# Kernel optimization log

Hardware: AMD Instinct MI355X
Metric: run time of the kernel (lower is better)

The kernel has to match this reference:

```python
import jax, jax.numpy as jnp
import numpy as np

B, DIM, H, W = 4, 192, 128, 128
HEADS = 4
K_RATES = (1.0 / 2, 2.0 / 3, 3.0 / 4, 4.0 / 5)


def setup_inputs() -> dict:
    key = jax.random.key(0)
    ks = jax.random.split(key, 5)
    x = jax.random.normal(ks[0], (B, DIM, H, W), jnp.float32)
    w_qkv = jax.random.normal(ks[1], (3 * DIM, DIM, 1, 1), jnp.float32) * 0.05
    w_dw = jax.random.normal(ks[2], (3 * DIM, 1, 3, 3), jnp.float32) * 0.05
    w_proj = jax.random.normal(ks[3], (DIM, DIM, 1, 1), jnp.float32) * 0.05
    temperature = jnp.ones((HEADS, 1, 1), jnp.float32)
    attn_w = jnp.full((4,), 0.2, jnp.float32)
    return {"x": x, "w_qkv": w_qkv, "w_dw": w_dw, "w_proj": w_proj,
            "temperature": temperature, "attn_w": attn_w}


def _conv1x1(x, w):
    # x: [b,c,h,w], w: [o,c,1,1]
    return jnp.einsum('bchw,oc->bohw', x, w[:, :, 0, 0])


def _dwconv3x3(x, w):
    # depthwise 3x3, padding=1; w: [c,1,3,3]
    return jax.lax.conv_general_dilated(
        x, w, window_strides=(1, 1), padding=((1, 1), (1, 1)),
        dimension_numbers=('NCHW', 'OIHW', 'NCHW'),
        feature_group_count=x.shape[1])


def _l2norm(x, eps=1e-12):
    # matches F.normalize(dim=-1): x / max(||x||, eps)
    n = jnp.sqrt(jnp.sum(x * x, axis=-1, keepdims=True))
    return x / jnp.maximum(n, eps)


def reference(x, w_qkv, w_dw, w_proj, temperature, attn_w):
    b, c, h, w = x.shape
    qkv = _dwconv3x3(_conv1x1(x, w_qkv), w_dw)  # [b, 3c, h, w]
    q, k, v = jnp.split(qkv, 3, axis=1)

    def heads(t):
        return t.reshape(b, HEADS, c // HEADS, h * w)  # [b, head, C, hw]

    q, k, v = heads(q), heads(k), heads(v)
    q = _l2norm(q)
    k = _l2norm(k)

    C = q.shape[2]
    attn = jnp.einsum('bhcn,bhdn->bhcd', q, k) * temperature[None]  # [b,head,C,C]

    out = jnp.zeros_like(v)
    for i, rate in enumerate(K_RATES):
        k_val = max(1, int(C * rate))
        _, idx = jax.lax.top_k(attn, k_val)  # [b,head,C,k]
        mask = jax.nn.one_hot(idx, C, dtype=attn.dtype).sum(axis=-2)  # [b,head,C,C]
        branch = jnp.where(mask > 0, attn, -jnp.inf)
        branch = jax.nn.softmax(branch, axis=-1)
        out = out + jnp.einsum('bhcd,bhdn->bhcn', branch, v) * attn_w[i]

    out = out.reshape(b, c, h, w)
    return _conv1x1(out, w_proj)
```

## Files before the change

kernel.cpp:

```cpp
#include <hip/hip_runtime.h>
#include <math.h>
#include <stdint.h>

#define BB 4
#define DIM 192
#define HEADS 4
#define CH 48
#define HW 16384
#define C3 576
#define NCHUNK 64

typedef unsigned short ushort_t;
typedef __attribute__((ext_vector_type(8))) short short8;
typedef __attribute__((ext_vector_type(4))) float floatx4;

__device__ __forceinline__ float bf2f(unsigned int u) {
    union { unsigned int i; float f; } v; v.i = u << 16; return v.f;
}
__device__ __forceinline__ ushort_t f2bf(float f) {
    union { float f; unsigned int i; } v; v.f = f;
    unsigned int x = v.i;
    x += 0x7fffu + ((x >> 16) & 1u);
    return (ushort_t)(x >> 16);
}

__global__ __launch_bounds__(256) void zero_init(float* __restrict__ p, int n) {
    int i = blockIdx.x * 256 + threadIdx.x;
    if (i < n) p[i] = 0.f;
}

__global__ __launch_bounds__(256) void convert_split(
    const float* __restrict__ in, ushort_t* __restrict__ hi,
    ushort_t* __restrict__ lo, int n)
{
    int i = blockIdx.x * 256 + threadIdx.x;
    if (i < n) {
        float f = in[i];
        ushort_t h = f2bf(f);
        hi[i] = h;
        lo[i] = f2bf(f - bf2f(h));
    }
}

__global__ __launch_bounds__(256) void tconv(
    const float* __restrict__ in, ushort_t* __restrict__ out_hi,
    ushort_t* __restrict__ out_lo, long inStride)
{
    int z = blockIdx.z;
    in += (long)z * inStride;
    out_hi += (long)z * HW * DIM;
    out_lo += (long)z * HW * DIM;
    __shared__ ushort_t th[64][80];
    __shared__ ushort_t tl[64][80];
    int n0 = blockIdx.x * 64, k0 = blockIdx.y * 64;
    int t = threadIdx.x;
#pragma unroll
    for (int i = 0; i < 4; ++i) {
        int kl = (t >> 4) + 16 * i;
        float4 v = *(const float4*)(in + (long)(k0 + kl) * HW + n0 + (t & 15) * 4);
        int nl = (t & 15) * 4;
        ushort_t hx = f2bf(v.x), hy = f2bf(v.y), hz = f2bf(v.z), hw = f2bf(v.w);
        th[nl + 0][kl] = hx; th[nl + 1][kl] = hy;
        th[nl + 2][kl] = hz; th[nl + 3][kl] = hw;
        tl[nl + 0][kl] = f2bf(v.x - bf2f(hx));
        tl[nl + 1][kl] = f2bf(v.y - bf2f(hy));
        tl[nl + 2][kl] = f2bf(v.z - bf2f(hz));
        tl[nl + 3][kl] = f2bf(v.w - bf2f(hw));
    }
    __syncthreads();
#pragma unroll
    for (int i = 0; i < 2; ++i) {
        int nl = t >> 2, seg = (t & 3) + 4 * i;
        *(uint4*)(out_hi + (long)(n0 + nl) * DIM + k0 + seg * 8) = *(uint4*)&th[nl][seg * 8];
        *(uint4*)(out_lo + (long)(n0 + nl) * DIM + k0 + seg * 8) = *(uint4*)&tl[nl][seg * 8];
    }
}

__global__ __launch_bounds__(256) void tconv_b16(
    const ushort_t* __restrict__ in, ushort_t* __restrict__ out)
{
    int z = blockIdx.z;
    in  += (long)z * DIM * HW;
    out += (long)z * HW * DIM;
    __shared__ ushort_t th[64][80];
    int n0 = blockIdx.x * 64, k0 = blockIdx.y * 64;
    int t = threadIdx.x;
#pragma unroll
    for (int i = 0; i < 4; ++i) {
        int kl = (t >> 4) + 16 * i;
        uint2 v = *(const uint2*)(in + (long)(k0 + kl) * HW + n0 + (t & 15) * 4);
        int nl = (t & 15) * 4;
        th[nl + 0][kl] = (ushort_t)(v.x & 0xffffu);
        th[nl + 1][kl] = (ushort_t)(v.x >> 16);
        th[nl + 2][kl] = (ushort_t)(v.y & 0xffffu);
        th[nl + 3][kl] = (ushort_t)(v.y >> 16);
    }
    __syncthreads();
#pragma unroll
    for (int i = 0; i < 2; ++i) {
        int nl = t >> 2, seg = (t & 3) + 4 * i;
        *(uint4*)(out + (long)(n0 + nl) * DIM + k0 + seg * 8) = *(uint4*)&th[nl][seg * 8];
    }
}

#define BS_STRIDE 104
template<int TERMS>
__global__ __launch_bounds__(256) void gemm_reg(
    const ushort_t* __restrict__ Ahi, const ushort_t* __restrict__ Alo,
    const ushort_t* __restrict__ BThi, const ushort_t* __restrict__ BTlo,
    float* __restrict__ C, int M, int N,
    long strideA, long strideB, long strideC)
{
    int z = blockIdx.z;
    Ahi += z * strideA; Alo += z * strideA;
    BThi += z * strideB; BTlo += z * strideB;
    C += z * strideC;
    __shared__ ushort_t Bs0[64 * BS_STRIDE];
    __shared__ ushort_t Bs1[64 * BS_STRIDE];
    int t = threadIdx.x;
    int wave = t >> 6, lane = t & 63;
    int l15 = lane & 15, quad = lane >> 4;
    int m0 = blockIdx.y * 64, n0 = blockIdx.x * 64;
    int wm = (wave & 1) * 32, wn = (wave >> 1) * 32;
    floatx4 acc[2][2];
#pragma unroll
    for (int i = 0; i < 2; ++i)
#pragma unroll
        for (int j = 0; j < 2; ++j) acc[i][j] = (floatx4){0.f, 0.f, 0.f, 0.f};

    if (TERMS == 1) {
        short8 af[2][6];
#pragma unroll
        for (int mi = 0; mi < 2; ++mi)
#pragma unroll
            for (int k0 = 0; k0 < 6; ++k0)
                af[mi][k0] = *(const short8*)(Ahi
                    + (long)(m0 + wm + mi * 16 + l15) * 192 + k0 * 32 + quad * 8);
        for (int i = t; i < 1536; i += 256) {
            int r = i / 24, seg = i % 24;
            uint4 v = *(const uint4*)(BThi + (long)(n0 + r) * 192 + seg * 8);
            ushort_t* dst = (seg < 12) ? &Bs0[r * BS_STRIDE + seg * 8]
                                       : &Bs1[r * BS_STRIDE + (seg - 12) * 8];
            *(uint4*)dst = v;
        }
        __syncthreads();
#pragma unroll
        for (int k0 = 0; k0 < 6; ++k0) {
            int ks = k0 * 32 + quad * 8;
            const ushort_t* buf = (ks < 96) ? Bs0 : Bs1;
            int col = (ks < 96) ? ks : ks - 96;
            short8 bf[2];
#pragma unroll
            for (int ni = 0; ni < 2; ++ni)
                bf[ni] = *(const short8*)&buf[(wn + ni * 16 + l15) * BS_STRIDE + col];
#pragma unroll
            for (int mi = 0; mi < 2; ++mi)
#pragma unroll
                for (int ni = 0; ni < 2; ++ni)
                    acc[mi][ni] = __builtin_amdgcn_mfma_f32_16x16x32_bf16(
                        af[mi][k0], bf[ni], acc[mi][ni], 0, 0, 0);
        }
    } else {
#pragma unroll
        for (int kh = 0; kh < 2; ++kh) {
            short8 ah[2][3], al[2][3];
#pragma unroll
            for (int mi = 0; mi < 2; ++mi)
#pragma unroll
                for (int k0 = 0; k0 < 3; ++k0) {
                    long off = (long)(m0 + wm + mi * 16 + l15) * 192
                             + kh * 96 + k0 * 32 + quad * 8;
                    ah[mi][k0] = *(const short8*)(Ahi + off);
                    al[mi][k0] = *(const short8*)(Alo + off);
                }
            if (kh) __syncthreads();
            for (int i = t; i < 768; i += 256) {
                int r = i / 12, seg = i % 12;
                long goff = (long)(n0 + r) * 192 + kh * 96 + seg * 8;
                *(uint4*)&Bs0[r * BS_STRIDE + seg * 8] = *(const uint4*)(BThi + goff);
                *(uint4*)&Bs1[r * BS_STRIDE + seg * 8] = *(const uint4*)(BTlo + goff);
            }
            __syncthreads();
#pragma unroll
            for (int k0 = 0; k0 < 3; ++k0) {
                int col = k0 * 32 + quad * 8;
                short8 bh[2], bl[2];
#pragma unroll
                for (int ni = 0; ni < 2; ++ni) {
                    bh[ni] = *(const short8*)&Bs0[(wn + ni * 16 + l15) * BS_STRIDE + col];
                    bl[ni] = *(const short8*)&Bs1[(wn + ni * 16 + l15) * BS_STRIDE + col];
                }
#pragma unroll
                for (int mi = 0; mi < 2; ++mi)
#pragma unroll
                    for (int ni = 0; ni < 2; ++ni) {
                        acc[mi][ni] = __builtin_amdgcn_mfma_f32_16x16x32_bf16(
                            ah[mi][k0], bh[ni], acc[mi][ni], 0, 0, 0);
                        acc[mi][ni] = __builtin_amdgcn_mfma_f32_16x16x32_bf16(
                            ah[mi][k0], bl[ni], acc[mi][ni], 0, 0, 0);
                        acc[mi][ni] = __builtin_amdgcn_mfma_f32_16x16x32_bf16(
                            al[mi][k0], bh[ni], acc[mi][ni], 0, 0, 0);
                    }
            }
        }
    }
#pragma unroll
    for (int mi = 0; mi < 2; ++mi)
#pragma unroll
        for (int ni = 0; ni < 2; ++ni) {
            long base = (long)(m0 + wm + mi * 16 + quad * 4) * N + n0 + wn + ni * 16 + l15;
#pragma unroll
            for (int r = 0; r < 4; ++r)
                C[base + (long)r * N] = acc[mi][ni][r];
        }
}

__global__ __launch_bounds__(256) void dwconv3x3_lds(
    const float* __restrict__ in, const float* __restrict__ w,
    ushort_t* __restrict__ qk_hi, ushort_t* __restrict__ qk_lo,
    ushort_t* __restrict__ vbuf16, float* __restrict__ normsq,
    int c0, int chunk)
{
    __shared__ float tile[10][132];
    int z = blockIdx.z;
    int cl = blockIdx.y;
    int gc = c0 + cl;
    in  += (long)z * chunk * HW + (long)cl * HW;
    int y0 = blockIdx.x * 8;
    const float* wc = w + gc * 9;
    float wf[9];
#pragma unroll
    for (int i = 0; i < 9; ++i) wf[i] = wc[i];
    int t = threadIdx.x;
    if (t < 10) { tile[t][0] = 0.f; tile[t][129] = 0.f; }
    for (int i = t; i < 320; i += 256) {
        int r = i >> 5, c4 = (i & 31) * 4;
        int gy = y0 - 1 + r;
        float4 v = {0.f, 0.f, 0.f, 0.f};
        if (gy >= 0 && gy < 128) v = *(const float4*)(in + gy * 128 + c4);
        tile[r][1 + c4] = v.x; tile[r][2 + c4] = v.y;
        tile[r][3 + c4] = v.z; tile[r][4 + c4] = v.w;
    }
    __syncthreads();
    int yl = t >> 5, xl = (t & 31) * 4;
    float s0 = 0.f, s1 = 0.f, s2 = 0.f, s3 = 0.f;
#pragma unroll
    for (int r = 0; r < 3; ++r) {
        float c0v = tile[yl + r][xl + 0], c1v = tile[yl + r][xl + 1];
        float c2v = tile[yl + r][xl + 2], c3v = tile[yl + r][xl + 3];
        float c4v = tile[yl + r][xl + 4], c5v = tile[yl + r][xl + 5];
        float w0 = wf[r * 3], w1 = wf[r * 3 + 1], w2 = wf[r * 3 + 2];
        s0 += w0 * c0v + w1 * c1v + w2 * c2v;
        s1 += w0 * c1v + w1 * c2v + w2 * c3v;
        s2 += w0 * c2v + w1 * c3v + w2 * c4v;
        s3 += w0 * c3v + w1 * c4v + w2 * c5v;
    }
    long pix = (long)(y0 + yl) * 128 + xl;
    ushort_t h0 = f2bf(s0), h1 = f2bf(s1), h2 = f2bf(s2), h3 = f2bf(s3);
    uint2 ph;
    ph.x = (unsigned)h0 | ((unsigned)h1 << 16);
    ph.y = (unsigned)h2 | ((unsigned)h3 << 16);
    if (gc < 2 * DIM) {
        ushort_t l0 = f2bf(s0 - bf2f(h0)), l1 = f2bf(s1 - bf2f(h1));
        ushort_t l2 = f2bf(s2 - bf2f(h2)), l3 = f2bf(s3 - bf2f(h3));
        uint2 pl;
        pl.x = (unsigned)l0 | ((unsigned)l1 << 16);
        pl.y = (unsigned)l2 | ((unsigned)l3 << 16);
        long rbase = ((long)z * 384 + gc) * HW + pix;
        *(uint2*)(qk_hi + rbase) = ph;
        *(uint2*)(qk_lo + rbase) = pl;
        __syncthreads();
        float* red = (float*)tile;
        red[t] = s0 * s0 + s1 * s1 + s2 * s2 + s3 * s3;
        __syncthreads();
        for (int off = 128; off > 0; off >>= 1) {
            if (t < off) red[t] += red[t + off];
            __syncthreads();
        }
        if (t == 0) atomicAdd(&normsq[z * 512 + gc], red[0]);
    } else {
        *(uint2*)(vbuf16 + ((long)z * DIM + (gc - 2 * DIM)) * HW + pix) = ph;
    }
}

__global__ __launch_bounds__(256) void attn_mfma(
    const ushort_t* __restrict__ qk_hi, const ushort_t* __restrict__ qk_lo,
    float* __restrict__ partial)
{
    int z = blockIdx.z, h = blockIdx.y, pidx = blockIdx.x;
    int t = threadIdx.x;
    int wave = t >> 6, lane = t & 63;
    int l15 = lane & 15, quad = lane >> 4;
    long base = (long)z * 384 * HW;
    const ushort_t* qh = qk_hi + base + (long)(h * CH) * HW;
    const ushort_t* ql = qk_lo + base + (long)(h * CH) * HW;
    const ushort_t* kh = qk_hi + base + (long)(DIM + h * CH) * HW;
    const ushort_t* kl = qk_lo + base + (long)(DIM + h * CH) * HW;
    int ncol0 = pidx * 256 + wave * 64;

    floatx4 acc[3][3];
#pragma unroll
    for (int i = 0; i < 3; ++i)
#pragma unroll
        for (int j = 0; j < 3; ++j) acc[i][j] = (floatx4){0.f, 0.f, 0.f, 0.f};

#pragma unroll
    for (int ks = 0; ks < 2; ++ks) {
        int col = ncol0 + ks * 32 + quad * 8;
        short8 ah[3], al[3], bh[3], bl[3];
#pragma unroll
        for (int i = 0; i < 3; ++i) {
            long ro = (long)(i * 16 + l15) * HW + col;
            ah[i] = *(const short8*)(qh + ro);
            al[i] = *(const short8*)(ql + ro);
            bh[i] = *(const short8*)(kh + ro);
            bl[i] = *(const short8*)(kl + ro);
        }
#pragma unroll
        for (int mi = 0; mi < 3; ++mi)
#pragma unroll
            for (int ni = 0; ni < 3; ++ni) {
                acc[mi][ni] = __builtin_amdgcn_mfma_f32_16x16x32_bf16(
                    ah[mi], bh[ni], acc[mi][ni], 0, 0, 0);
                acc[mi][ni] = __builtin_amdgcn_mfma_f32_16x16x32_bf16(
                    ah[mi], bl[ni], acc[mi][ni], 0, 0, 0);
                acc[mi][ni] = __builtin_amdgcn_mfma_f32_16x16x32_bf16(
                    al[mi], bh[ni], acc[mi][ni], 0, 0, 0);
            }
    }

    __shared__ float sred[2][48 * 50];
    float* sb = sred[wave & 1];
    if (wave < 2) {
#pragma unroll
        for (int mi = 0; mi < 3; ++mi)
#pragma unroll
            for (int ni = 0; ni < 3; ++ni)
#pragma unroll
                for (int r = 0; r < 4; ++r)
                    sb[(mi * 16 + quad * 4 + r) * 50 + ni * 16 + l15] = acc[mi][ni][r];
    }
    __syncthreads();
    if (wave >= 2) {
#pragma unroll
        for (int mi = 0; mi < 3; ++mi)
#pragma unroll
            for (int ni = 0; ni < 3; ++ni)
#pragma unroll
                for (int r = 0; r < 4; ++r)
                    sb[(mi * 16 + quad * 4 + r) * 50 + ni * 16 + l15] += acc[mi][ni][r];
    }
    __syncthreads();
    float* pp = partial + ((long)(pidx * 16 + z * HEADS + h)) * 2304;
    for (int i = t; i < 2304; i += 256) {
        int row = i / 48, colo = i - row * 48;
        pp[i] = sred[0][row * 50 + colo] + sred[1][row * 50 + colo];
    }
}

__global__ __launch_bounds__(256) void topk_combine2(
    const float* __restrict__ partial, const float* __restrict__ normsq,
    const float* __restrict__ temp, const float* __restrict__ attn_w,
    float* __restrict__ Wc)
{
    int z = blockIdx.y;
    int wave = threadIdx.x >> 6, lane = threadIdx.x & 63;
    int rid = blockIdx.x * 4 + wave;
    int c = rid % CH, h = rid / CH;
    int d = lane;
    float a = -INFINITY;
    if (d < 48) {
        float s = 0.f;
        const float* pp = partial + (long)(z * HEADS + h) * 2304 + c * CH + d;
        for (int p = 0; p < NCHUNK; ++p) s += pp[(long)p * 16 * 2304];
        float invq = 1.0f / fmaxf(sqrtf(normsq[z * 512 + h * CH + c]), 1e-12f);
        float invk = 1.0f / fmaxf(sqrtf(normsq[z * 512 + DIM + h * CH + d]), 1e-12f);
        a = s * invq * invk * temp[h];
    }
    float m = a;
#pragma unroll
    for (int off = 32; off > 0; off >>= 1) m = fmaxf(m, __shfl_xor(m, off, 64));
    float e = (d < 48) ? expf(a - m) : 0.f;
    int rank = 0;
    for (int j = 0; j < 48; ++j) {
        float aj = __shfl(a, j, 64);
        rank += (aj > a) || (aj == a && j < d);
    }
    const int kv[4] = {24, 32, 36, 38};
    float s = 0.f;
#pragma unroll
    for (int i = 0; i < 4; ++i) {
        float contrib = (d < 48 && rank < kv[i]) ? e : 0.f;
#pragma unroll
        for (int off = 32; off > 0; off >>= 1) contrib += __shfl_xor(contrib, off, 64);
        s += (rank < kv[i]) ? attn_w[i] / contrib : 0.f;
    }
    if (d < 48) Wc[(long)z * 9216 + (long)rid * CH + d] = e * s;
}

__global__ __launch_bounds__(256) void build_m(
    const float* __restrict__ wproj, const float* __restrict__ Wc,
    ushort_t* __restrict__ Mb)
{
    int z = blockIdx.y;
    int idx = blockIdx.x * 256 + threadIdx.x;
    if (idx >= DIM * DIM) return;
    int cg = idx % DIM;
    int o  = idx / DIM;
    int h = cg / CH, d = cg % CH;
    const float* wp = wproj + o * DIM + h * CH;
    const float* wcc = Wc + (long)z * 9216 + (long)h * CH * CH + d;
    float s = 0.f;
#pragma unroll
    for (int ch = 0; ch < CH; ++ch) s += wp[ch] * wcc[ch * CH];
    Mb[(long)z * DIM * DIM + idx] = f2bf(s);
}

extern "C" void kernel_launch(void* const* d_in, const int* in_sizes, int n_in,
                              void* d_out, int out_size, void* d_ws, size_t ws_size,
                              hipStream_t stream) {
    const float* x      = (const float*)d_in[0];
    const float* w_qkv  = (const float*)d_in[1];
    const float* w_dw   = (const float*)d_in[2];
    const float* w_proj = (const float*)d_in[3];
    const float* temper = (const float*)d_in[4];
    const float* attn_w = (const float*)d_in[5];
    float* out = (float*)d_out;

    char* p = (char*)d_ws;
    ushort_t* qk_hi  = (ushort_t*)p;   p += (long)BB * 384 * HW * 2;
    ushort_t* qk_lo  = (ushort_t*)p;   p += (long)BB * 384 * HW * 2;
    ushort_t* vbuf16 = (ushort_t*)p;   p += (long)BB * DIM * HW * 2;
    ushort_t* xT_hi  = (ushort_t*)p;   p += (long)BB * HW * DIM * 2;
    ushort_t* xT_lo  = (ushort_t*)p;   p += (long)BB * HW * DIM * 2;
    ushort_t* wq_hi  = (ushort_t*)p;   p += (long)C3 * DIM * 2;
    ushort_t* wq_lo  = (ushort_t*)p;   p += (long)C3 * DIM * 2;
    float* normsq    = (float*)p;      p += (long)BB * 512 * 4;
    float* Wc        = (float*)p;      p += (long)BB * 9216 * 4;
    ushort_t* Mb     = (ushort_t*)p;   p += (long)BB * DIM * DIM * 2;
    float* pre       = (float*)p;
    float* partial   = pre;
    long avail = (long)ws_size - (long)(p - (char*)d_ws);
    int chunk = 64;
    if (avail >= (long)BB * 192 * HW * 4) chunk = 192;

    zero_init<<<(BB * 512 + 255) / 256, 256, 0, stream>>>(normsq, BB * 512);
    convert_split<<<(C3 * DIM + 255) / 256, 256, 0, stream>>>(
        w_qkv, wq_hi, wq_lo, C3 * DIM);
    tconv<<<dim3(HW / 64, DIM / 64, BB), 256, 0, stream>>>(
        x, xT_hi, xT_lo, (long)DIM * HW);

    for (int c0 = 0; c0 < C3; c0 += chunk) {
        if (c0 < 2 * DIM)
            gemm_reg<3><<<dim3(HW / 64, chunk / 64, BB), 256, 0, stream>>>(
                wq_hi + (long)c0 * DIM, wq_lo + (long)c0 * DIM, xT_hi, xT_lo,
                pre, chunk, HW, 0L, (long)HW * DIM, (long)chunk * HW);
        else
            gemm_reg<1><<<dim3(HW / 64, chunk / 64, BB), 256, 0, stream>>>(
                wq_hi + (long)c0 * DIM, wq_hi + (long)c0 * DIM, xT_hi, xT_hi,
                pre, chunk, HW, 0L, (long)HW * DIM, (long)chunk * HW);
        dwconv3x3_lds<<<dim3(16, chunk, BB), 256, 0, stream>>>(
            pre, w_dw, qk_hi, qk_lo, vbuf16, normsq, c0, chunk);
    }
    attn_mfma<<<dim3(NCHUNK, HEADS, BB), 256, 0, stream>>>(qk_hi, qk_lo, partial);
    topk_combine2<<<dim3(48, BB), 256, 0, stream>>>(
        partial, normsq, temper, attn_w, Wc);
    build_m<<<dim3((DIM * DIM + 255) / 256, BB), 256, 0, stream>>>(w_proj, Wc, Mb);
    tconv_b16<<<dim3(HW / 64, DIM / 64, BB), 256, 0, stream>>>(vbuf16, xT_hi);
    gemm_reg<1><<<dim3(HW / 64, DIM / 64, BB), 256, 0, stream>>>(
        Mb, Mb, xT_hi, xT_hi, out, DIM, HW,
        (long)DIM * DIM, (long)HW * DIM, (long)DIM * HW);
}
```

Measured before the change: 392.6 us.

## Drop LDS staging in gemm_reg, load B fragments directly, widen N tile

The GEMM no longer stages B tiles through shared memory with barriers. Each wave now reads its B fragments straight from global memory into registers. The block's N tile doubles to 128 (each wave covers 64 columns, with 2x4 accumulators) and grid sizes are halved to match. This removes LDS traffic and __syncthreads, at the cost of uncoalesced-ish 16-byte global reads per lane, more register pressure from the larger accumulator and fragment arrays, and fewer blocks.

New measurement: 413.9 us. 1.05x slower.

```diff
diff --git a/kernel.cpp b/kernel.cpp
--- a/kernel.cpp
+++ b/kernel.cpp
@@ -103,7 +103,6 @@
     }
 }
 
-#define BS_STRIDE 104
 template<int TERMS>
 __global__ __launch_bounds__(256) void gemm_reg(
     const ushort_t* __restrict__ Ahi, const ushort_t* __restrict__ Alo,
@@ -115,18 +114,34 @@
     Ahi += z * strideA; Alo += z * strideA;
     BThi += z * strideB; BTlo += z * strideB;
     C += z * strideC;
-    __shared__ ushort_t Bs0[64 * BS_STRIDE];
-    __shared__ ushort_t Bs1[64 * BS_STRIDE];
     int t = threadIdx.x;
     int wave = t >> 6, lane = t & 63;
     int l15 = lane & 15, quad = lane >> 4;
-    int m0 = blockIdx.y * 64, n0 = blockIdx.x * 64;
-    int wm = (wave & 1) * 32, wn = (wave >> 1) * 32;
-    floatx4 acc[2][2];
+    int m0 = blockIdx.y * 64, n0 = blockIdx.x * 128;
+    int wm = (wave & 1) * 32, wn = (wave >> 1) * 64;
+
+    const ushort_t* bph[4];
+    const ushort_t* bpl[4];
+#pragma unroll
+    for (int ni = 0; ni < 4; ++ni) {
+        long ro = (long)(n0 + wn + ni * 16 + l15) * 192;
+        bph[ni] = BThi + ro;
+        bpl[ni] = BTlo + ro;
+    }
+    const ushort_t* aph[2];
+    const ushort_t* apl[2];
+#pragma unroll
+    for (int mi = 0; mi < 2; ++mi) {
+        long ro = (long)(m0 + wm + mi * 16 + l15) * 192;
+        aph[mi] = Ahi + ro;
+        apl[mi] = Alo + ro;
+    }
+
+    floatx4 acc[2][4];
 #pragma unroll
     for (int i = 0; i < 2; ++i)
 #pragma unroll
-        for (int j = 0; j < 2; ++j) acc[i][j] = (floatx4){0.f, 0.f, 0.f, 0.f};
+        for (int j = 0; j < 4; ++j) acc[i][j] = (floatx4){0.f, 0.f, 0.f, 0.f};
 
     if (TERMS == 1) {
         short8 af[2][6];
@@ -134,29 +149,18 @@
         for (int mi = 0; mi < 2; ++mi)
 #pragma unroll
             for (int k0 = 0; k0 < 6; ++k0)
-                af[mi][k0] = *(const short8*)(Ahi
-                    + (long)(m0 + wm + mi * 16 + l15) * 192 + k0 * 32 + quad * 8);
-        for (int i = t; i < 1536; i += 256) {
-            int r = i / 24, seg = i % 24;
-            uint4 v = *(const uint4*)(BThi + (long)(n0 + r) * 192 + seg * 8);
-            ushort_t* dst = (seg < 12) ? &Bs0[r * BS_STRIDE + seg * 8]
-                                       : &Bs1[r * BS_STRIDE + (seg - 12) * 8];
-            *(uint4*)dst = v;
-        }
-        __syncthreads();
+                af[mi][k0] = *(const short8*)(aph[mi] + k0 * 32 + quad * 8);
 #pragma unroll
         for (int k0 = 0; k0 < 6; ++k0) {
-            int ks = k0 * 32 + quad * 8;
-            const ushort_t* buf = (ks < 96) ? Bs0 : Bs1;
-            int col = (ks < 96) ? ks : ks - 96;
-            short8 bf[2];
-#pragma unroll
-            for (int ni = 0; ni < 2; ++ni)
-                bf[ni] = *(const short8*)&buf[(wn + ni * 16 + l15) * BS_STRIDE + col];
+            int col = k0 * 32 + quad * 8;
+            short8 bf[4];
+#pragma unroll
+            for (int ni = 0; ni < 4; ++ni)
+                bf[ni] = *(const short8*)(bph[ni] + col);
 #pragma unroll
             for (int mi = 0; mi < 2; ++mi)
 #pragma unroll
-                for (int ni = 0; ni < 2; ++ni)
+                for (int ni = 0; ni < 4; ++ni)
                     acc[mi][ni] = __builtin_amdgcn_mfma_f32_16x16x32_bf16(
                         af[mi][k0], bf[ni], acc[mi][ni], 0, 0, 0);
         }
@@ -168,32 +172,23 @@
             for (int mi = 0; mi < 2; ++mi)
 #pragma unroll
                 for (int k0 = 0; k0 < 3; ++k0) {
-                    long off = (long)(m0 + wm + mi * 16 + l15) * 192
-                             + kh * 96 + k0 * 32 + quad * 8;
-                    ah[mi][k0] = *(const short8*)(Ahi + off);
-                    al[mi][k0] = *(const short8*)(Alo + off);
+                    int col = kh * 96 + k0 * 32 + quad * 8;
+                    ah[mi][k0] = *(const short8*)(aph[mi] + col);
+                    al[mi][k0] = *(const short8*)(apl[mi] + col);
                 }
-            if (kh) __syncthreads();
-            for (int i = t; i < 768; i += 256) {
-                int r = i / 12, seg = i % 12;
-                long goff = (long)(n0 + r) * 192 + kh * 96 + seg * 8;
-                *(uint4*)&Bs0[r * BS_STRIDE + seg * 8] = *(const uint4*)(BThi + goff);
-                *(uint4*)&Bs1[r * BS_STRIDE + seg * 8] = *(const uint4*)(BTlo + goff);
-            }
-            __syncthreads();
 #pragma unroll
             for (int k0 = 0; k0 < 3; ++k0) {
-                int col = k0 * 32 + quad * 8;
-                short8 bh[2], bl[2];
-#pragma unroll
-                for (int ni = 0; ni < 2; ++ni) {
-                    bh[ni] = *(const short8*)&Bs0[(wn + ni * 16 + l15) * BS_STRIDE + col];
-                    bl[ni] = *(const short8*)&Bs1[(wn + ni * 16 + l15) * BS_STRIDE + col];
+                int col = kh * 96 + k0 * 32 + quad * 8;
+                short8 bh[4], bl[4];
+#pragma unroll
+                for (int ni = 0; ni < 4; ++ni) {
+                    bh[ni] = *(const short8*)(bph[ni] + col);
+                    bl[ni] = *(const short8*)(bpl[ni] + col);
                 }
 #pragma unroll
                 for (int mi = 0; mi < 2; ++mi)
 #pragma unroll
-                    for (int ni = 0; ni < 2; ++ni) {
+                    for (int ni = 0; ni < 4; ++ni) {
                         acc[mi][ni] = __builtin_amdgcn_mfma_f32_16x16x32_bf16(
                             ah[mi][k0], bh[ni], acc[mi][ni], 0, 0, 0);
                         acc[mi][ni] = __builtin_amdgcn_mfma_f32_16x16x32_bf16(
@@ -207,7 +202,7 @@
 #pragma unroll
     for (int mi = 0; mi < 2; ++mi)
 #pragma unroll
-        for (int ni = 0; ni < 2; ++ni) {
+        for (int ni = 0; ni < 4; ++ni) {
             long base = (long)(m0 + wm + mi * 16 + quad * 4) * N + n0 + wn + ni * 16 + l15;
 #pragma unroll
             for (int r = 0; r < 4; ++r)
@@ -452,11 +447,11 @@
 
     for (int c0 = 0; c0 < C3; c0 += chunk) {
         if (c0 < 2 * DIM)
-            gemm_reg<3><<<dim3(HW / 64, chunk / 64, BB), 256, 0, stream>>>(
+            gemm_reg<3><<<dim3(HW / 128, chunk / 64, BB), 256, 0, stream>>>(
                 wq_hi + (long)c0 * DIM, wq_lo + (long)c0 * DIM, xT_hi, xT_lo,
                 pre, chunk, HW, 0L, (long)HW * DIM, (long)chunk * HW);
         else
-            gemm_reg<1><<<dim3(HW / 64, chunk / 64, BB), 256, 0, stream>>>(
+            gemm_reg<1><<<dim3(HW / 128, chunk / 64, BB), 256, 0, stream>>>(
                 wq_hi + (long)c0 * DIM, wq_hi + (long)c0 * DIM, xT_hi, xT_hi,
                 pre, chunk, HW, 0L, (long)HW * DIM, (long)chunk * HW);
         dwconv3x3_lds<<<dim3(16, chunk, BB), 256, 0, stream>>>(
@@ -467,7 +462,7 @@
         partial, normsq, temper, attn_w, Wc);
     build_m<<<dim3((DIM * DIM + 255) / 256, BB), 256, 0, stream>>>(w_proj, Wc, Mb);
     tconv_b16<<<dim3(HW / 64, DIM / 64, BB), 256, 0, stream>>>(vbuf16, xT_hi);
-    gemm_reg<1><<<dim3(HW / 64, DIM / 64, BB), 256, 0, stream>>>(
+    gemm_reg<1><<<dim3(HW / 128, DIM / 64, BB), 256, 0, stream>>>(
         Mb, Mb, xT_hi, xT_hi, out, DIM, HW,
         (long)DIM * DIM, (long)HW * DIM, (long)DIM * HW);
 }
```
